# Kernel tuning notes

Hardware: AMD Instinct MI355X
Metric: run time of the kernel (lower is better)

The kernel has to match this reference:

```python
import jax, jax.numpy as jnp
import numpy as np

T, S, W, D, C, K = 16, 16, 10, 512, 64, 512  # tasks, shots, ways, z_dim, n_concept, triplets/group


def setup_inputs() -> dict:
    key = jax.random.key(0)
    ks = jax.random.split(key, 12)
    sc = 0.02
    inp = {
        "input_data": jax.random.normal(ks[0], (T, S, W, D), dtype=jnp.float32),
        "triplet_idx": jax.random.randint(ks[1], (T, W, 3, K), 0, S * W, dtype=jnp.int64),
        # proj_inner: Linear(3D -> 2D), ReLU, Linear(2D -> D)
        "W1": jax.random.normal(ks[2], (3 * D, 2 * D), dtype=jnp.float32) * sc,
        "b1": jnp.zeros((2 * D,), dtype=jnp.float32),
        "W2": jax.random.normal(ks[3], (2 * D, D), dtype=jnp.float32) * sc,
        "b2": jnp.zeros((D,), dtype=jnp.float32),
        # proj_outer: Linear(D -> 2D), ReLU, Linear(2D -> D)
        "W3": jax.random.normal(ks[4], (D, 2 * D), dtype=jnp.float32) * sc,
        "b3": jnp.zeros((2 * D,), dtype=jnp.float32),
        "W4": jax.random.normal(ks[5], (2 * D, D), dtype=jnp.float32) * sc,
        "b4": jnp.zeros((D,), dtype=jnp.float32),
        # cls: Linear(D -> C)
        "Wc": jax.random.normal(ks[6], (D, C), dtype=jnp.float32) * sc,
        "bc": jnp.zeros((C,), dtype=jnp.float32),
    }
    return inp


def reference(input_data, triplet_idx, W1, b1, W2, b2, W3, b3, W4, b4, Wc, bc):
    t, s, w, d = input_data.shape
    x = input_data.reshape(t, s * w, d)                     # [T, N, D], N = shot*way
    # gather triplet embeddings: [T, W, 3, K, D]
    emb = x[jnp.arange(t)[:, None, None, None], triplet_idx]
    # permute([1,0,2]).reshape(-1, 3*dim): [T, W, K, 3*D]
    trip = jnp.swapaxes(emb, 2, 3).reshape(t, w, -1, 3 * d)
    # proj_inner MLP then sum over triplets
    h = jax.nn.relu(trip @ W1 + b1) @ W2 + b2               # [T, W, K, D]
    g = jnp.sum(h, axis=2)                                  # [T, W, D]
    # proj_outer MLP -> cls -> softmax
    o = jax.nn.relu(g @ W3 + b3) @ W4 + b4                  # [T, W, D]
    score = o @ Wc + bc                                     # [T, W, C]
    return jax.nn.softmax(score, axis=-1)
```

## Files before the change

### kernel.cpp

```cpp
#include <hip/hip_runtime.h>
#include <hip/hip_bf16.h>

#define T_  16
#define W_  10
#define D_  512
#define SW_ 160
#define N1_ 1024
#define KT_ 512

typedef __bf16 bf16x8 __attribute__((ext_vector_type(8)));
typedef _Float16 f16x8 __attribute__((ext_vector_type(8)));
typedef _Float16 h2v  __attribute__((ext_vector_type(2)));
typedef float  f32x4  __attribute__((ext_vector_type(4)));

__device__ __forceinline__ void async16(const void* g, void* l) {
  __builtin_amdgcn_global_load_lds(
      (__attribute__((address_space(1))) void*)(g),
      (__attribute__((address_space(3))) void*)(l), 16, 0, 0);
}

__device__ __forceinline__ h2v bc2(unsigned u) { return __builtin_bit_cast(h2v, u); }
__device__ __forceinline__ h2v relu2(h2v a) {
  h2v r;
  asm("v_pk_max_f16 %0, %1, 0" : "=v"(r) : "v"(a));
  return r;
}

__global__ __launch_bounds__(256) void prep_all(
    const float* __restrict__ x_in, const float* __restrict__ W1,
    const float* __restrict__ W2, const float* __restrict__ W3,
    const float* __restrict__ W4, const float* __restrict__ Wc,
    const float* __restrict__ b2, const float* __restrict__ b3,
    const float* __restrict__ b4, const float* __restrict__ bc,
    __hip_bfloat16* __restrict__ xbf, __hip_bfloat16* __restrict__ w1t,
    _Float16* __restrict__ w2b, _Float16* __restrict__ w3t,
    _Float16* __restrict__ w4b, _Float16* __restrict__ wct,
    float* __restrict__ b23, float* __restrict__ bc4)
{
  __shared__ float tile[32 * 33];
  const int b = blockIdx.x, tid = threadIdx.x;

  auto cast4h = [&](const float* src, _Float16* dst, int base) {
    int i = (base + tid) << 2;
    float4 v = *(const float4*)(src + i);
    __align__(8) _Float16 o4[4] = {(_Float16)v.x, (_Float16)v.y,
                                   (_Float16)v.z, (_Float16)v.w};
    *(uint2*)(dst + i) = *(const uint2*)o4;
  };
  auto tr32h = [&](const float* src, _Float16* dst, int R, int C, int rt, int ct) {
    int r0 = rt << 5, c0 = ct << 5;
    int c = tid & 31, rr = tid >> 5;
#pragma unroll
    for (int i = 0; i < 4; ++i) {
      int r = rr + i * 8;
      tile[r * 33 + c] = src[(size_t)(r0 + r) * C + c0 + c];
    }
    __syncthreads();
#pragma unroll
    for (int i = 0; i < 4; ++i) {
      int r = rr + i * 8;
      dst[(size_t)(c0 + r) * R + r0 + c] = (_Float16)tile[c * 33 + r];
    }
  };

  if (b < 1280) {
    int i = (b * 256 + tid) << 2;
    float4 v = *(const float4*)(x_in + i);
    __align__(8) __hip_bfloat16 o4[4];
    o4[0] = __float2bfloat16(v.x); o4[1] = __float2bfloat16(v.y);
    o4[2] = __float2bfloat16(v.z); o4[3] = __float2bfloat16(v.w);
    *(uint2*)(xbf + i) = *(const uint2*)o4;
  } else if (b < 2816) {
    int q = b - 1280;
    int r0 = (q >> 5) << 5, c0 = (q & 31) << 5;
    int c = tid & 31, rr = tid >> 5;
#pragma unroll
    for (int i = 0; i < 4; ++i) {
      int r = rr + i * 8;
      tile[r * 33 + c] = W1[(size_t)(r0 + r) * 1024 + c0 + c];
    }
    __syncthreads();
#pragma unroll
    for (int i = 0; i < 4; ++i) {
      int r = rr + i * 8;
      w1t[(size_t)(c0 + r) * 1536 + r0 + c] = __float2bfloat16(tile[c * 33 + r]);
    }
  } else if (b < 3328) {
    cast4h(W2, w2b, (b - 2816) * 256);
  } else if (b < 3840) {
    int q = b - 3328; tr32h(W3, w3t, 512, 1024, q >> 5, q & 31);
  } else if (b < 4352) {
    cast4h(W4, w4b, (b - 3840) * 256);
  } else if (b < 4384) {
    int q = b - 4352; tr32h(Wc, wct, 512, 64, q >> 1, q & 1);
  } else if (b < 4388) {
    int c = (b - 4384) * 256 + tid;
    float s = 0.f;
#pragma unroll 32
    for (int j = 0; j < 512; ++j) s += b2[j] * W3[(size_t)j * 1024 + c];
    b23[c] = 512.f * s + b3[c];
  } else {
    if (tid < 64) {
      float s = 0.f;
#pragma unroll 32
      for (int j = 0; j < 512; ++j) s += b4[j] * Wc[(size_t)j * 64 + tid];
      bc4[tid] = s + bc[tid];
    }
  }
}

__global__ __launch_bounds__(256) void group_wgemm(
    const __hip_bfloat16* __restrict__ xbf,
    const __hip_bfloat16* __restrict__ w1t,
    const int* __restrict__ tidx,
    const float* __restrict__ b1,
    _Float16* __restrict__ Hsb,
    const _Float16* __restrict__ w3t,
    const _Float16* __restrict__ w2b,
    const _Float16* __restrict__ wct,
    const _Float16* __restrict__ w4b,
    _Float16* __restrict__ w23t,
    _Float16* __restrict__ w4ct)
{
  __shared__ __align__(16) char smem[65536];
  const int bx = blockIdx.x;
  const int tid = threadIdx.x;
  const int ln = tid & 63, wv = tid >> 6;
  const int col16 = ln & 15, quad = ln >> 4;

  if (bx >= 512) {
    const int b = bx - 512;
    const _Float16 *A, *Bt;
    _Float16* out;
    int m0, n0;
    if (b < 256) { A = w3t; Bt = w2b; out = w23t; m0 = (b >> 4) << 6; n0 = (b & 15) << 6; }
    else         { A = wct; Bt = w4b; out = w4ct; m0 = 0;             n0 = (b - 256) << 6; }
    char* Abuf = smem;
    char* Bbuf = smem + 16384;

    f32x4 acc[4];
#pragma unroll
    for (int a = 0; a < 4; ++a) acc[a] = (f32x4){0.f, 0.f, 0.f, 0.f};

#pragma unroll 1
    for (int kk = 0; kk < 512; kk += 128) {
      __syncthreads();
#pragma unroll
      for (int p = 0; p < 4; ++p) {
        int i = p * 256 + tid, r = i >> 4, q = i & 15;
        async16(A + (size_t)(m0 + r) * 512 + kk + ((q ^ (r & 7)) << 3), Abuf + (i << 4));
      }
#pragma unroll
      for (int p = 0; p < 4; ++p) {
        int i = p * 256 + tid, r = i >> 4, q = i & 15;
        async16(Bt + (size_t)(n0 + r) * 512 + kk + ((q ^ (r & 7)) << 3), Bbuf + (i << 4));
      }
      __syncthreads();

#pragma unroll
      for (int ks = 0; ks < 4; ++ks) {
        const int qq = (ks << 2) + quad;
        const int rn = (wv << 4) + col16;
        f16x8 bfm = *(const f16x8*)(Bbuf + rn * 256 + ((qq ^ (rn & 7)) << 4));
#pragma unroll
        for (int a = 0; a < 4; ++a) {
          int rm = (a << 4) + col16;
          f16x8 af = *(const f16x8*)(Abuf + rm * 256 + ((qq ^ (rm & 7)) << 4));
          acc[a] = __builtin_amdgcn_mfma_f32_16x16x32_f16(af, bfm, acc[a], 0, 0, 0);
        }
      }
    }

    const int n = n0 + (wv << 4) + col16;
#pragma unroll
    for (int a = 0; a < 4; ++a)
#pragma unroll
      for (int r = 0; r < 4; ++r) {
        size_t row = m0 + (a << 4) + (quad << 2) + r;
        out[row * 1024 + n] = (_Float16)acc[a][r];
      }
    return;
  }

  char* Abuf  = smem;
  char* Bbuf  = smem + 40960;
  char* Ptile = smem;
  int*  ibuf  = (int*)(smem + 34560);
  float* red  = (float*)(smem + 59136);

  const int t   = bx >> 5;
  const int nt  = bx & 31;
  const int n0  = nt << 5;

  const int wr = wv >> 1, wc = wv & 1;

  const __hip_bfloat16* xt = xbf + (size_t)t * (SW_ * D_);

  int aoff[10], lofA[10];
#pragma unroll
  for (int s = 0; s < 10; ++s) {
    int i = s * 256 + tid, r = i >> 4, q = i & 15;
    aoff[s] = r * 512 + ((q ^ (r & 7)) << 3);
    lofA[s] = i << 4;
  }
  int boff[6], lofB[6];
#pragma unroll
  for (int s = 0; s < 6; ++s) {
    int i = s * 256 + tid, r = i >> 4, q = i & 15;
    int nc = r & 31, j = r >> 5;
    boff[s] = (n0 + nc) * 1536 + j * 512 + ((q ^ (r & 7)) << 3);
    lofB[s] = i << 4;
  }

  f32x4 acc[5][3];
#pragma unroll
  for (int a = 0; a < 5; ++a)
#pragma unroll
    for (int b = 0; b < 3; ++b)
      acc[a][b] = (f32x4){0.f, 0.f, 0.f, 0.f};

#pragma unroll 1
  for (int kk = 0; kk < 512; kk += 128) {
    __syncthreads();
#pragma unroll
    for (int s = 0; s < 10; ++s) async16(xt + aoff[s] + kk, Abuf + lofA[s]);
#pragma unroll
    for (int s = 0; s < 6; ++s) async16(w1t + boff[s] + kk, Bbuf + lofB[s]);
    __syncthreads();

#pragma unroll
    for (int ks = 0; ks < 4; ++ks) {
      const int qq = (ks << 2) + quad;
      bf16x8 af[5], bfr[3];
#pragma unroll
      for (int a = 0; a < 5; ++a) {
        int rm = wr * 80 + a * 16 + col16;
        af[a] = *(const bf16x8*)(Abuf + rm * 256 + ((qq ^ (rm & 7)) << 4));
      }
#pragma unroll
      for (int b = 0; b < 3; ++b) {
        int rn = wc * 48 + b * 16 + col16;
        bfr[b] = *(const bf16x8*)(Bbuf + rn * 256 + ((qq ^ (rn & 7)) << 4));
      }
#pragma unroll
      for (int a = 0; a < 5; ++a)
#pragma unroll
        for (int b = 0; b < 3; ++b)
          acc[a][b] = __builtin_amdgcn_mfma_f32_16x16x32_bf16(af[a], bfr[b], acc[a][b], 0, 0, 0);
    }
  }

  __syncthreads();

#pragma unroll
  for (int b = 0; b < 3; ++b) {
    int c = wc * 48 + b * 16 + col16;
    int j = c >> 5, nc = c & 31;
    float bv = (j == 2) ? b1[n0 + nc] : 0.f;
#pragma unroll
    for (int a = 0; a < 5; ++a) {
      int mb = wr * 80 + a * 16 + quad * 4;
#pragma unroll
      for (int r = 0; r < 4; ++r)
        *(_Float16*)(Ptile + (j * 160 + mb + r) * 72 + nc * 2) =
            (_Float16)(acc[a][b][r] + bv);
    }
  }

  const int nq = tid & 7;
  const int kq = tid >> 3;
  const char* Pt0 = Ptile + (nq << 3);
  const char* Pt1 = Pt0 + 11520;
  const char* Pt2 = Pt0 + 23040;

  const int* tsrc = tidx + (size_t)t * 10 * 1536;
  int4 ra[2], rb[2];
  auto sst2 = [&](int* dstbase) {
#pragma unroll
    for (int v = 0; v < 2; ++v) {
      int* dst = dstbase + v * 1536;
      *(int4*)(dst + (tid << 2)) =
          make_int4(ra[v].x * 72, ra[v].y * 72, ra[v].z * 72, ra[v].w * 72);
      if (tid < 128)
        *(int4*)(dst + 1024 + (tid << 2)) =
            make_int4(rb[v].x * 72, rb[v].y * 72, rb[v].z * 72, rb[v].w * 72);
    }
  };

#pragma unroll
  for (int v = 0; v < 2; ++v) {
    const int* s0 = tsrc + v * 1536;
    ra[v] = *(const int4*)(s0 + (tid << 2));
    if (tid < 128) rb[v] = *(const int4*)(s0 + 1024 + (tid << 2));
  }
  sst2(ibuf);
  int cur = 0;

#pragma unroll 1
  for (int wp = 0; wp < 5; ++wp) {
    __syncthreads();
    if (wp < 4) {
#pragma unroll
      for (int v = 0; v < 2; ++v) {
        const int* s2 = tsrc + (wp * 2 + 2 + v) * 1536;
        ra[v] = *(const int4*)(s2 + (tid << 2));
        if (tid < 128) rb[v] = *(const int4*)(s2 + 1024 + (tid << 2));
      }
    }

    const int* cb = ibuf + cur * 3072;
    f32x4 a4[2];
#pragma unroll
    for (int v = 0; v < 2; ++v) {
      const int* cid = cb + v * 1536;
      h2v acc01 = (h2v)0, acc23 = (h2v)0;
#pragma unroll
      for (int u = 0; u < 4; ++u) {
        const int kb = (kq << 4) + (u << 2);
        int4 i0 = *(const int4*)(cid + kb);
        int4 i1 = *(const int4*)(cid + 512 + kb);
        int4 i2 = *(const int4*)(cid + 1024 + kb);
#define STEP(IA, IB, IC)                                                  \
        {                                                                 \
          uint2 p0 = *(const uint2*)(Pt0 + (IA));                         \
          uint2 p1 = *(const uint2*)(Pt1 + (IB));                         \
          uint2 p2 = *(const uint2*)(Pt2 + (IC));                         \
          h2v sx = bc2(p0.x) + bc2(p1.x) + bc2(p2.x);                     \
          h2v sy = bc2(p0.y) + bc2(p1.y) + bc2(p2.y);                     \
          acc01 += relu2(sx);                                             \
          acc23 += relu2(sy);                                             \
        }
        STEP(i0.x, i1.x, i2.x)
        STEP(i0.y, i1.y, i2.y)
        STEP(i0.z, i1.z, i2.z)
        STEP(i0.w, i1.w, i2.w)
#undef STEP
      }
      a4[v] = (f32x4){(float)acc01.x, (float)acc01.y,
                      (float)acc23.x, (float)acc23.y};
    }

    if (wp < 4) sst2(ibuf + (cur ^ 1) * 3072);

#pragma unroll
    for (int v = 0; v < 2; ++v) {
#pragma unroll
      for (int off = 8; off <= 32; off <<= 1) {
        a4[v].x += __shfl_xor(a4[v].x, off);
        a4[v].y += __shfl_xor(a4[v].y, off);
        a4[v].z += __shfl_xor(a4[v].z, off);
        a4[v].w += __shfl_xor(a4[v].w, off);
      }
      if ((ln >> 3) == 0)
        *(f32x4*)(red + v * 128 + wv * 32 + (nq << 2)) = a4[v];
    }
    __syncthreads();
    if (tid < 64) {
      int v = tid >> 5, c = tid & 31;
      const float* rv = red + v * 128;
      float s = rv[c] + rv[32 + c] + rv[64 + c] + rv[96 + c];
      Hsb[(size_t)(t * 10 + wp * 2 + v) * N1_ + n0 + c] = (_Float16)s;
    }
    cur ^= 1;
  }
}

__global__ __launch_bounds__(256) void mid_head(
    const _Float16* __restrict__ A,
    const _Float16* __restrict__ Bt,
    const _Float16* __restrict__ W4c,
    const float* __restrict__ bias,
    float* __restrict__ psc)
{
  __shared__ __align__(16) char Abuf[40960];
  __shared__ __align__(16) char Bbuf[32768];
  __shared__ __align__(16) char Hbuf[8192];
  const int tid = threadIdx.x;
  const int n0 = blockIdx.x << 6;
  const int m0 = blockIdx.y * 80;
  const int ln = tid & 63, wv = tid >> 6;
  const int col16 = ln & 15, quad = ln >> 4;

#pragma unroll
  for (int p = 0; p < 2; ++p) {
    int i = p * 256 + tid, r = i >> 3, q = i & 7;
    async16(W4c + (size_t)r * 1024 + n0 + ((q ^ (r & 7)) << 3), Hbuf + (i << 4));
  }

  f32x4 acc[5];
#pragma unroll
  for (int a = 0; a < 5; ++a) acc[a] = (f32x4){0.f, 0.f, 0.f, 0.f};

#pragma unroll 1
  for (int kk = 0; kk < 1024; kk += 256) {
    __syncthreads();
#pragma unroll
    for (int p = 0; p < 10; ++p) {
      int i = p * 256 + tid, r = i >> 5, q = i & 31;
      async16(A + (size_t)(m0 + r) * 1024 + kk + ((q ^ (r & 7)) << 3), Abuf + (i << 4));
    }
#pragma unroll
    for (int p = 0; p < 8; ++p) {
      int i = p * 256 + tid, r = i >> 5, q = i & 31;
      async16(Bt + (size_t)(n0 + r) * 1024 + kk + ((q ^ (r & 7)) << 3), Bbuf + (i << 4));
    }
    __syncthreads();

#pragma unroll
    for (int ks = 0; ks < 8; ++ks) {
      const int qq = (ks << 2) + quad;
      const int rn = (wv << 4) + col16;
      f16x8 bfm = *(const f16x8*)(Bbuf + rn * 512 + ((qq ^ (rn & 7)) << 4));
#pragma unroll
      for (int a = 0; a < 5; ++a) {
        int rm = (a << 4) + col16;
        f16x8 af = *(const f16x8*)(Abuf + rm * 512 + ((qq ^ (rm & 7)) << 4));
        acc[a] = __builtin_amdgcn_mfma_f32_16x16x32_f16(af, bfm, acc[a], 0, 0, 0);
      }
    }
  }

  const float bb = bias[n0 + (wv << 4) + col16];
  __syncthreads();
  char* U = Abuf;
  const int cl = (wv << 4) + col16;
#pragma unroll
  for (int a = 0; a < 5; ++a)
#pragma unroll
    for (int r = 0; r < 4; ++r) {
      float v = fmaxf(acc[a][r] + bb, 0.f);
      int m = (a << 4) + (quad << 2) + r;
      *(_Float16*)(U + m * 128 + (((cl >> 3) ^ (m & 7)) << 4) + ((cl & 7) << 1)) =
          (_Float16)v;
    }
  __syncthreads();

  f32x4 acc2[5];
#pragma unroll
  for (int a = 0; a < 5; ++a) acc2[a] = (f32x4){0.f, 0.f, 0.f, 0.f};
#pragma unroll
  for (int ks = 0; ks < 2; ++ks) {
    const int qq = (ks << 2) + quad;
    const int rn = (wv << 4) + col16;
    f16x8 bfm = *(const f16x8*)(Hbuf + rn * 128 + ((qq ^ (rn & 7)) << 4));
#pragma unroll
    for (int a = 0; a < 5; ++a) {
      int rm = (a << 4) + col16;
      f16x8 af = *(const f16x8*)(U + rm * 128 + ((qq ^ (rm & 7)) << 4));
      acc2[a] = __builtin_amdgcn_mfma_f32_16x16x32_f16(af, bfm, acc2[a], 0, 0, 0);
    }
  }
  float* po = psc + ((size_t)blockIdx.x * 160 + m0) * 64;
#pragma unroll
  for (int a = 0; a < 5; ++a)
#pragma unroll
    for (int r = 0; r < 4; ++r)
      po[((a << 4) + (quad << 2) + r) * 64 + (wv << 4) + col16] = acc2[a][r];
}

__global__ __launch_bounds__(256) void softmax2(
    const float* __restrict__ psc,
    const float* __restrict__ bc4,
    float* __restrict__ out)
{
  __shared__ float sc[80 * 64];
  __shared__ float rs[80];
  const int tid = threadIdx.x;
  const int m0 = blockIdx.x * 80;

#pragma unroll
  for (int p = 0; p < 5; ++p) {
    int f = p * 256 + tid;
    int r = f >> 4, cq = f & 15;
    f32x4 s = (f32x4){0.f, 0.f, 0.f, 0.f};
#pragma unroll
    for (int j = 0; j < 16; ++j)
      s += *(const f32x4*)(psc + ((size_t)(j * 160) + m0 + r) * 64 + (cq << 2));
    s += *(const f32x4*)(bc4 + (cq << 2));
    *(f32x4*)(sc + r * 64 + (cq << 2)) = s;
  }
  __syncthreads();

  if (tid < 80) {
    float m = -1e30f;
    for (int c = 0; c < 64; ++c) m = fmaxf(m, sc[tid * 64 + c]);
    float s = 0.f;
    for (int c = 0; c < 64; ++c) {
      float e = expf(sc[tid * 64 + c] - m);
      sc[tid * 64 + c] = e;
      s += e;
    }
    rs[tid] = 1.f / s;
  }
  __syncthreads();
#pragma unroll
  for (int p = 0; p < 20; ++p) {
    int f = p * 256 + tid, r = f >> 6, c = f & 63;
    out[(size_t)(m0 + r) * 64 + c] = sc[f] * rs[r];
  }
}

extern "C" void kernel_launch(void* const* d_in, const int* in_sizes, int n_in,
                              void* d_out, int out_size, void* d_ws, size_t ws_size,
                              hipStream_t stream) {
  const float* x_in = (const float*)d_in[0];
  const int*   tidx = (const int*)d_in[1];
  const float* W1 = (const float*)d_in[2];
  const float* b1 = (const float*)d_in[3];
  const float* W2 = (const float*)d_in[4];
  const float* b2 = (const float*)d_in[5];
  const float* W3 = (const float*)d_in[6];
  const float* b3 = (const float*)d_in[7];
  const float* W4 = (const float*)d_in[8];
  const float* b4 = (const float*)d_in[9];
  const float* Wc = (const float*)d_in[10];
  const float* bc = (const float*)d_in[11];
  float* out = (float*)d_out;
  (void)in_sizes; (void)n_in; (void)out_size; (void)ws_size;

  char* ws = (char*)d_ws;
  __hip_bfloat16* xbf  = (__hip_bfloat16*)(ws + 0);
  __hip_bfloat16* w1t  = (__hip_bfloat16*)(ws + 2621440);
  _Float16*       w2b  = (_Float16*)      (ws + 5767168);
  _Float16*       w3t  = (_Float16*)      (ws + 6815744);
  _Float16*       w4b  = (_Float16*)      (ws + 7864320);
  _Float16*       wct  = (_Float16*)      (ws + 8912896);
  float*          b23  = (float*)         (ws + 8978432);
  float*          bc4  = (float*)         (ws + 8982528);
  _Float16*       Hsb  = (_Float16*)      (ws + 8982784);
  _Float16*       w23t = (_Float16*)      (ws + 9310464);
  _Float16*       w4ct = (_Float16*)      (ws + 11407616);
  float*          psc  = (float*)         (ws + 11538688);

  prep_all<<<4389, 256, 0, stream>>>(x_in, W1, W2, W3, W4, Wc, b2, b3, b4, bc,
                                     xbf, w1t, w2b, w3t, w4b, wct, b23, bc4);

  group_wgemm<<<784, 256, 0, stream>>>(xbf, w1t, tidx, b1, Hsb,
                                       w3t, w2b, wct, w4b, w23t, w4ct);

  mid_head<<<dim3(16, 2), 256, 0, stream>>>(Hsb, w23t, w4ct, b23, psc);

  softmax2<<<2, 256, 0, stream>>>(psc, bc4, out);
}
```

Measured before the change: 146.7 us.

## Shrink group GEMM LDS tile and precompute scaled triplet indices in prep

Halves the K-step of the triplet-projection GEMM so shared memory drops to about 34 KB, and requests three blocks per SM through launch bounds. Triplet indices are pre-scaled by the P-tile row stride in the prep kernel and read straight from global memory. This replaces the double-buffered index staging in LDS and the cross-wave reduction with one wave per group and shuffle-only reductions. The aim is higher occupancy and fewer block barriers, at the cost of twice as many K-loop iterations and barriers, plus uncached global index loads in the gather loop.

```diff
diff --git a/kernel.cpp b/kernel.cpp
--- a/kernel.cpp
+++ b/kernel.cpp
@@ -32,10 +32,12 @@
     const float* __restrict__ W4, const float* __restrict__ Wc,
     const float* __restrict__ b2, const float* __restrict__ b3,
     const float* __restrict__ b4, const float* __restrict__ bc,
+    const int* __restrict__ tidx,
     __hip_bfloat16* __restrict__ xbf, __hip_bfloat16* __restrict__ w1t,
     _Float16* __restrict__ w2b, _Float16* __restrict__ w3t,
     _Float16* __restrict__ w4b, _Float16* __restrict__ wct,
-    float* __restrict__ b23, float* __restrict__ bc4)
+    float* __restrict__ b23, float* __restrict__ bc4,
+    int* __restrict__ idx72)
 {
   __shared__ float tile[32 * 33];
   const int b = blockIdx.x, tid = threadIdx.x;
@@ -99,20 +101,24 @@
 #pragma unroll 32
     for (int j = 0; j < 512; ++j) s += b2[j] * W3[(size_t)j * 1024 + c];
     b23[c] = 512.f * s + b3[c];
-  } else {
+  } else if (b < 4389) {
     if (tid < 64) {
       float s = 0.f;
 #pragma unroll 32
       for (int j = 0; j < 512; ++j) s += b4[j] * Wc[(size_t)j * 64 + tid];
       bc4[tid] = s + bc[tid];
     }
-  }
-}
-
-__global__ __launch_bounds__(256) void group_wgemm(
+  } else {
+    int i = ((b - 4389) * 256 + tid) << 2;
+    int4 v = *(const int4*)(tidx + i);
+    *(int4*)(idx72 + i) = make_int4(v.x * 72, v.y * 72, v.z * 72, v.w * 72);
+  }
+}
+
+__global__ __launch_bounds__(256, 3) void group_wgemm(
     const __hip_bfloat16* __restrict__ xbf,
     const __hip_bfloat16* __restrict__ w1t,
-    const int* __restrict__ tidx,
+    const int* __restrict__ idx72,
     const float* __restrict__ b1,
     _Float16* __restrict__ Hsb,
     const _Float16* __restrict__ w3t,
@@ -122,7 +128,7 @@
     _Float16* __restrict__ w23t,
     _Float16* __restrict__ w4ct)
 {
-  __shared__ __align__(16) char smem[65536];
+  __shared__ __align__(16) char smem[34560];
   const int bx = blockIdx.x;
   const int tid = threadIdx.x;
   const int ln = tid & 63, wv = tid >> 6;
@@ -183,10 +189,8 @@
   }
 
   char* Abuf  = smem;
-  char* Bbuf  = smem + 40960;
+  char* Bbuf  = smem + 20480;
   char* Ptile = smem;
-  int*  ibuf  = (int*)(smem + 34560);
-  float* red  = (float*)(smem + 59136);
 
   const int t   = bx >> 5;
   const int nt  = bx & 31;
@@ -196,17 +200,17 @@
 
   const __hip_bfloat16* xt = xbf + (size_t)t * (SW_ * D_);
 
-  int aoff[10], lofA[10];
-#pragma unroll
-  for (int s = 0; s < 10; ++s) {
-    int i = s * 256 + tid, r = i >> 4, q = i & 15;
+  int aoff[5], lofA[5];
+#pragma unroll
+  for (int s = 0; s < 5; ++s) {
+    int i = s * 256 + tid, r = i >> 3, q = i & 7;
     aoff[s] = r * 512 + ((q ^ (r & 7)) << 3);
     lofA[s] = i << 4;
   }
-  int boff[6], lofB[6];
-#pragma unroll
-  for (int s = 0; s < 6; ++s) {
-    int i = s * 256 + tid, r = i >> 4, q = i & 15;
+  int boff[3], lofB[3];
+#pragma unroll
+  for (int s = 0; s < 3; ++s) {
+    int i = s * 256 + tid, r = i >> 3, q = i & 7;
     int nc = r & 31, j = r >> 5;
     boff[s] = (n0 + nc) * 1536 + j * 512 + ((q ^ (r & 7)) << 3);
     lofB[s] = i << 4;
@@ -220,27 +224,27 @@
       acc[a][b] = (f32x4){0.f, 0.f, 0.f, 0.f};
 
 #pragma unroll 1
-  for (int kk = 0; kk < 512; kk += 128) {
+  for (int kk = 0; kk < 512; kk += 64) {
     __syncthreads();
 #pragma unroll
-    for (int s = 0; s < 10; ++s) async16(xt + aoff[s] + kk, Abuf + lofA[s]);
-#pragma unroll
-    for (int s = 0; s < 6; ++s) async16(w1t + boff[s] + kk, Bbuf + lofB[s]);
+    for (int s = 0; s < 5; ++s) async16(xt + aoff[s] + kk, Abuf + lofA[s]);
+#pragma unroll
+    for (int s = 0; s < 3; ++s) async16(w1t + boff[s] + kk, Bbuf + lofB[s]);
     __syncthreads();
 
 #pragma unroll
-    for (int ks = 0; ks < 4; ++ks) {
+    for (int ks = 0; ks < 2; ++ks) {
       const int qq = (ks << 2) + quad;
       bf16x8 af[5], bfr[3];
 #pragma unroll
       for (int a = 0; a < 5; ++a) {
         int rm = wr * 80 + a * 16 + col16;
-        af[a] = *(const bf16x8*)(Abuf + rm * 256 + ((qq ^ (rm & 7)) << 4));
+        af[a] = *(const bf16x8*)(Abuf + rm * 128 + ((qq ^ (rm & 7)) << 4));
       }
 #pragma unroll
       for (int b = 0; b < 3; ++b) {
         int rn = wc * 48 + b * 16 + col16;
-        bfr[b] = *(const bf16x8*)(Bbuf + rn * 256 + ((qq ^ (rn & 7)) << 4));
+        bfr[b] = *(const bf16x8*)(Bbuf + rn * 128 + ((qq ^ (rn & 7)) << 4));
       }
 #pragma unroll
       for (int a = 0; a < 5; ++a)
@@ -266,60 +270,29 @@
             (_Float16)(acc[a][b][r] + bv);
     }
   }
-
-  const int nq = tid & 7;
-  const int kq = tid >> 3;
+  __syncthreads();
+
+  const int kq8 = ln >> 3, nq = ln & 7;
   const char* Pt0 = Ptile + (nq << 3);
   const char* Pt1 = Pt0 + 11520;
   const char* Pt2 = Pt0 + 23040;
-
-  const int* tsrc = tidx + (size_t)t * 10 * 1536;
-  int4 ra[2], rb[2];
-  auto sst2 = [&](int* dstbase) {
-#pragma unroll
-    for (int v = 0; v < 2; ++v) {
-      int* dst = dstbase + v * 1536;
-      *(int4*)(dst + (tid << 2)) =
-          make_int4(ra[v].x * 72, ra[v].y * 72, ra[v].z * 72, ra[v].w * 72);
-      if (tid < 128)
-        *(int4*)(dst + 1024 + (tid << 2)) =
-            make_int4(rb[v].x * 72, rb[v].y * 72, rb[v].z * 72, rb[v].w * 72);
-    }
-  };
-
-#pragma unroll
-  for (int v = 0; v < 2; ++v) {
-    const int* s0 = tsrc + v * 1536;
-    ra[v] = *(const int4*)(s0 + (tid << 2));
-    if (tid < 128) rb[v] = *(const int4*)(s0 + 1024 + (tid << 2));
-  }
-  sst2(ibuf);
-  int cur = 0;
+  const int* ibase = idx72 + (size_t)t * 10 * 1536 + (kq8 << 6);
 
 #pragma unroll 1
-  for (int wp = 0; wp < 5; ++wp) {
-    __syncthreads();
-    if (wp < 4) {
-#pragma unroll
-      for (int v = 0; v < 2; ++v) {
-        const int* s2 = tsrc + (wp * 2 + 2 + v) * 1536;
-        ra[v] = *(const int4*)(s2 + (tid << 2));
-        if (tid < 128) rb[v] = *(const int4*)(s2 + 1024 + (tid << 2));
-      }
-    }
-
-    const int* cb = ibuf + cur * 3072;
-    f32x4 a4[2];
-#pragma unroll
-    for (int v = 0; v < 2; ++v) {
-      const int* cid = cb + v * 1536;
+  for (int w = wv; w < 10; w += 4) {
+    const int* c0 = ibase + w * 1536;
+    const int* c1 = c0 + 512;
+    const int* c2 = c0 + 1024;
+    f32x4 a4 = (f32x4){0.f, 0.f, 0.f, 0.f};
+#pragma unroll
+    for (int c4 = 0; c4 < 4; ++c4) {
       h2v acc01 = (h2v)0, acc23 = (h2v)0;
 #pragma unroll
       for (int u = 0; u < 4; ++u) {
-        const int kb = (kq << 4) + (u << 2);
-        int4 i0 = *(const int4*)(cid + kb);
-        int4 i1 = *(const int4*)(cid + 512 + kb);
-        int4 i2 = *(const int4*)(cid + 1024 + kb);
+        const int off = (c4 << 4) + (u << 2);
+        int4 i0 = *(const int4*)(c0 + off);
+        int4 i1 = *(const int4*)(c1 + off);
+        int4 i2 = *(const int4*)(c2 + off);
 #define STEP(IA, IB, IC)                                                  \
         {                                                                 \
           uint2 p0 = *(const uint2*)(Pt0 + (IA));                         \
@@ -336,32 +309,23 @@
         STEP(i0.w, i1.w, i2.w)
 #undef STEP
       }
-      a4[v] = (f32x4){(float)acc01.x, (float)acc01.y,
-                      (float)acc23.x, (float)acc23.y};
-    }
-
-    if (wp < 4) sst2(ibuf + (cur ^ 1) * 3072);
-
-#pragma unroll
-    for (int v = 0; v < 2; ++v) {
-#pragma unroll
-      for (int off = 8; off <= 32; off <<= 1) {
-        a4[v].x += __shfl_xor(a4[v].x, off);
-        a4[v].y += __shfl_xor(a4[v].y, off);
-        a4[v].z += __shfl_xor(a4[v].z, off);
-        a4[v].w += __shfl_xor(a4[v].w, off);
-      }
-      if ((ln >> 3) == 0)
-        *(f32x4*)(red + v * 128 + wv * 32 + (nq << 2)) = a4[v];
-    }
-    __syncthreads();
-    if (tid < 64) {
-      int v = tid >> 5, c = tid & 31;
-      const float* rv = red + v * 128;
-      float s = rv[c] + rv[32 + c] + rv[64 + c] + rv[96 + c];
-      Hsb[(size_t)(t * 10 + wp * 2 + v) * N1_ + n0 + c] = (_Float16)s;
-    }
-    cur ^= 1;
+      a4.x += (float)acc01.x; a4.y += (float)acc01.y;
+      a4.z += (float)acc23.x; a4.w += (float)acc23.y;
+    }
+
+#pragma unroll
+    for (int off = 8; off <= 32; off <<= 1) {
+      a4.x += __shfl_xor(a4.x, off);
+      a4.y += __shfl_xor(a4.y, off);
+      a4.z += __shfl_xor(a4.z, off);
+      a4.w += __shfl_xor(a4.w, off);
+    }
+    if (kq8 == 0) {
+      __align__(8) _Float16 o4[4] = {(_Float16)a4.x, (_Float16)a4.y,
+                                     (_Float16)a4.z, (_Float16)a4.w};
+      *(uint2*)(Hsb + (size_t)(t * 10 + w) * N1_ + n0 + (nq << 2)) =
+          *(const uint2*)o4;
+    }
   }
 }
 
@@ -531,11 +495,12 @@
   _Float16*       w23t = (_Float16*)      (ws + 9310464);
   _Float16*       w4ct = (_Float16*)      (ws + 11407616);
   float*          psc  = (float*)         (ws + 11538688);
-
-  prep_all<<<4389, 256, 0, stream>>>(x_in, W1, W2, W3, W4, Wc, b2, b3, b4, bc,
-                                     xbf, w1t, w2b, w3t, w4b, wct, b23, bc4);
-
-  group_wgemm<<<784, 256, 0, stream>>>(xbf, w1t, tidx, b1, Hsb,
+  int*            idx72= (int*)           (ws + 12194048);
+
+  prep_all<<<4629, 256, 0, stream>>>(x_in, W1, W2, W3, W4, Wc, b2, b3, b4, bc, tidx,
+                                     xbf, w1t, w2b, w3t, w4b, wct, b23, bc4, idx72);
+
+  group_wgemm<<<784, 256, 0, stream>>>(xbf, w1t, idx72, b1, Hsb,
                                        w3t, w2b, wct, w4b, w23t, w4ct);
 
   mid_head<<<dim3(16, 2), 256, 0, stream>>>(Hsb, w23t, w4ct, b23, psc);
```

New measurement: 140.4 us (median of 2 runs). -4.3%, faster.
